# Kernel tuning notes

Measured on AMD Instinct MI355X. Metric: run time of the kernel, lower is better.

## Reference

```python
import jax, jax.numpy as jnp
import numpy as np

EPS = 1e-8  # torch.cosine_similarity default eps


def setup_inputs() -> dict:
    key = jax.random.key(0)
    ks = jax.random.split(key, 6)
    B, U, P, H = 256, 128, 64, 768
    utt_output = jax.random.normal(ks[0], (U, B, H), dtype=jnp.float32)
    pheno_output = jax.random.normal(ks[1], (P, B, H), dtype=jnp.float32)
    # Conv1d(in=U, out=U, kernel=P) weight: [out, in, kernel]
    w_utt = jax.random.normal(ks[2], (U, U, P), dtype=jnp.float32) / np.sqrt(U * P)
    b_utt = jax.random.normal(ks[3], (U,), dtype=jnp.float32) * 0.01
    # Conv1d(in=P, out=P, kernel=U) weight: [out, in, kernel]
    w_pheno = jax.random.normal(ks[4], (P, P, U), dtype=jnp.float32) / np.sqrt(P * U)
    b_pheno = jax.random.normal(ks[5], (P,), dtype=jnp.float32) * 0.01
    return {"utt_output": utt_output, "pheno_output": pheno_output,
            "w_utt": w_utt, "b_utt": b_utt, "w_pheno": w_pheno, "b_pheno": b_pheno}


def reference(utt_output, pheno_output, w_utt, b_utt, w_pheno, b_pheno):
    # [len, B, H] -> [B, len, H]
    u = jnp.swapaxes(utt_output, 0, 1)    # [B, U, H]
    p = jnp.swapaxes(pheno_output, 0, 1)  # [B, P, H]
    # cosine similarity matrix c[b,i,j] = <u_i, p_j> / (max(|u_i|,eps)*max(|p_j|,eps))
    un = u / jnp.maximum(jnp.linalg.norm(u, axis=-1, keepdims=True), EPS)
    pn = p / jnp.maximum(jnp.linalg.norm(p, axis=-1, keepdims=True), EPS)
    c = jnp.einsum('buh,bph->bup', un, pn)  # [B, U, P]
    # Conv1d with kernel covering the full width -> output length 1, i.e. an einsum
    row_logits = jnp.einsum('bup,oup->bo', c, w_utt) + b_utt        # [B, U]
    col_logits = jnp.einsum('bup,opu->bo', c, w_pheno) + b_pheno    # [B, P]
    row_attention = jax.nn.softmax(row_logits, axis=-1)
    col_attention = jax.nn.softmax(col_logits, axis=-1)
    return row_attention, col_attention
```

## Files before the change

### kernel.cpp

```cpp
#include <hip/hip_runtime.h>
#include <stdint.h>

#define Bn 256
#define Un 128
#define Pn 64
#define Hn 768
#define Ototal 192
#define KC 16

#define LDU 40
#define LDB 72

typedef short s4v __attribute__((ext_vector_type(4)));
typedef short s8v __attribute__((ext_vector_type(8)));
typedef float f4v __attribute__((ext_vector_type(4)));

__device__ __forceinline__ short f2bf(float x) {
  union { float f; uint32_t u; } c; c.f = x;
  uint32_t r = (c.u + 0x7fffu + ((c.u >> 16) & 1u)) >> 16;
  return (short)(r & 0xffffu);
}

__global__ void __launch_bounds__(256) convW(const float* __restrict__ w_utt,
                                             const float* __restrict__ w_ph,
                                             ushort* __restrict__ Wbf) {
  __shared__ float tile[64 * 129];
  const int bx = blockIdx.x;
  const int t = threadIdx.x;
  if (bx < 4096) {
    int idx = bx * 256 + t;
    Wbf[idx] = (ushort)f2bf(w_utt[idx]);
    return;
  }
  const int oc = bx - 4096;
  const float* src = w_ph + (size_t)oc * 8192;
#pragma unroll
  for (int itr = 0; itr < 8; ++itr) {
    int idx = itr * 1024 + t * 4;
    int j = idx >> 7, i = idx & 127;
    float4 v = *(const float4*)(src + idx);
    tile[j * 129 + i + 0] = v.x;
    tile[j * 129 + i + 1] = v.y;
    tile[j * 129 + i + 2] = v.z;
    tile[j * 129 + i + 3] = v.w;
  }
  __syncthreads();
  const size_t obase = (size_t)(128 + oc) * 8192;
#pragma unroll
  for (int itr = 0; itr < 8; ++itr) {
    int k = itr * 1024 + t * 4;
    int i = k >> 6, j = k & 63;
    s4v o4 = { f2bf(tile[(j + 0) * 129 + i]),
               f2bf(tile[(j + 1) * 129 + i]),
               f2bf(tile[(j + 2) * 129 + i]),
               f2bf(tile[(j + 3) * 129 + i]) };
    *(s4v*)&Wbf[obase + k] = o4;
  }
}

__global__ void __launch_bounds__(512) phaseA(const float* __restrict__ utt,
                                              const float* __restrict__ ph,
                                              ushort* __restrict__ Cbf) {
  const int bx = blockIdx.x;
  const int b = bx >> 1, half = bx & 1;
  const int t = threadIdx.x;
  const int w = t >> 6, l = t & 63;

  __shared__ short uA[64 * LDU];
  __shared__ short pB[64 * LDU];
  __shared__ float s_inu[64];
  __shared__ float s_inp[64];

  const int r  = t >> 3;
  const int cc = (t & 7) * 4;

  const size_t rstride = (size_t)Bn * Hn;
  const float* ubase = utt + (size_t)b * Hn + (size_t)(half * 64 + r) * rstride + cc;
  const float* pbase = ph  + (size_t)b * Hn + (size_t)r * rstride + cc;

  float4 ru = *(const float4*)ubase;
  float4 rp = *(const float4*)pbase;

  float ssu = 0.f, ssp = 0.f;
  f4v zero4 = {0.f, 0.f, 0.f, 0.f};
  f4v acc0 = zero4, acc1 = zero4;

  const int m  = l & 15;
  const int ko = (l >> 4) * 8;
  const int it = w & 3;
  const int jp = w >> 2;
  const int lw = r * LDU + (t & 7) * 4;

  const short* ab = &uA[(it * 16 + m) * LDU + ko];
  const short* bb = &pB[(jp * 32 + m) * LDU + ko];

  for (int c = 0; c < 24; ++c) {
    __syncthreads();
    float4 a = ru, p0 = rp;
    ssu += a.x*a.x + a.y*a.y + a.z*a.z + a.w*a.w;
    ssp += p0.x*p0.x + p0.y*p0.y + p0.z*p0.z + p0.w*p0.w;
    s4v au = { f2bf(a.x),  f2bf(a.y),  f2bf(a.z),  f2bf(a.w)  };
    s4v pp = { f2bf(p0.x), f2bf(p0.y), f2bf(p0.z), f2bf(p0.w) };
    *(s4v*)&uA[lw] = au;
    *(s4v*)&pB[lw] = pp;
    __syncthreads();
    if (c < 23) {
      ru = *(const float4*)(ubase + (c + 1) * 32);
      rp = *(const float4*)(pbase + (c + 1) * 32);
    }
    s8v af  = *(const s8v*)ab;
    s8v bf0 = *(const s8v*)bb;
    s8v bf1 = *(const s8v*)(bb + 16 * LDU);
    acc0 = __builtin_amdgcn_mfma_f32_16x16x32_bf16(af, bf0, acc0, 0, 0, 0);
    acc1 = __builtin_amdgcn_mfma_f32_16x16x32_bf16(af, bf1, acc1, 0, 0, 0);
  }

  ssu += __shfl_xor(ssu, 4); ssu += __shfl_xor(ssu, 2); ssu += __shfl_xor(ssu, 1);
  ssp += __shfl_xor(ssp, 4); ssp += __shfl_xor(ssp, 2); ssp += __shfl_xor(ssp, 1);
  if ((t & 7) == 0) {
    s_inu[r] = 1.f / fmaxf(sqrtf(ssu), 1e-8f);
    s_inp[r] = 1.f / fmaxf(sqrtf(ssp), 1e-8f);
  }
  __syncthreads();

  const int cl = l & 15;
  const int rq = (l >> 4) * 4;
#pragma unroll
  for (int jt = 0; jt < 2; ++jt) {
    int j = jp * 32 + jt * 16 + cl;
    float sj = s_inp[j];
    f4v a = (jt == 0) ? acc0 : acc1;
#pragma unroll
    for (int rr = 0; rr < 4; ++rr) {
      int il = it * 16 + rq + rr;
      float v = a[rr] * s_inu[il] * sj;
      Cbf[((size_t)b * Un + half * 64 + il) * Pn + j] = (ushort)f2bf(v);
    }
  }
}

__global__ void __launch_bounds__(256) phaseB(const ushort* __restrict__ Cbf,
                                              const ushort* __restrict__ Wbf,
                                              float* __restrict__ partial) {
  const int kc = blockIdx.x;
  const int mt = blockIdx.y;
  const int nt = blockIdx.z;
  const int t = threadIdx.x;
  const int w = t >> 6, l = t & 63;

  __shared__ short Ab[64 * LDB];
  __shared__ short Bb[64 * LDB];

  const int row = t >> 2;
  const int k16 = (t & 3) * 16;

  f4v zero4 = {0.f, 0.f, 0.f, 0.f};
  f4v acc[4] = {zero4, zero4, zero4, zero4};

  const ushort* Ag = Cbf + (size_t)(mt * 64 + row) * 8192 + kc * 512 + k16;
  const ushort* Bg = Wbf + (size_t)(nt * 64 + row) * 8192 + kc * 512 + k16;
  const int m  = l & 15;
  const int ko = (l >> 4) * 8;

  for (int c = 0; c < 8; ++c) {
    s8v av0 = *(const s8v*)(Ag + c * 64);
    s8v av1 = *(const s8v*)(Ag + c * 64 + 8);
    s8v bv0 = *(const s8v*)(Bg + c * 64);
    s8v bv1 = *(const s8v*)(Bg + c * 64 + 8);
    __syncthreads();
    *(s8v*)&Ab[row * LDB + k16]     = av0;
    *(s8v*)&Ab[row * LDB + k16 + 8] = av1;
    *(s8v*)&Bb[row * LDB + k16]     = bv0;
    *(s8v*)&Bb[row * LDB + k16 + 8] = bv1;
    __syncthreads();
#pragma unroll
    for (int ks = 0; ks < 2; ++ks) {
      s8v af = *(const s8v*)&Ab[(16 * w + m) * LDB + ks * 32 + ko];
#pragma unroll
      for (int jt = 0; jt < 4; ++jt) {
        s8v bf = *(const s8v*)&Bb[(16 * jt + m) * LDB + ks * 32 + ko];
        acc[jt] = __builtin_amdgcn_mfma_f32_16x16x32_bf16(af, bf, acc[jt], 0, 0, 0);
      }
    }
  }

  const int rq = (l >> 4) * 4;
#pragma unroll
  for (int jt = 0; jt < 4; ++jt) {
    int og = nt * 64 + 16 * jt + (l & 15);
#pragma unroll
    for (int r = 0; r < 4; ++r) {
      int bg = mt * 64 + 16 * w + rq + r;
      partial[((size_t)kc * Bn + bg) * Ototal + og] = acc[jt][r];
    }
  }
}

__global__ void __launch_bounds__(192) phaseC(const float* __restrict__ partial,
                                              const float* __restrict__ b_utt,
                                              const float* __restrict__ b_ph,
                                              float* __restrict__ out) {
  const int b = blockIdx.x;
  const int t = threadIdx.x;
  const int w = t >> 6, l = t & 63;

  float v = 0.f;
#pragma unroll
  for (int kc = 0; kc < KC; ++kc)
    v += partial[((size_t)kc * Bn + b) * Ototal + t];
  v += (t < Un) ? b_utt[t] : b_ph[t - Un];

  __shared__ float red[3];
  float mx = v;
  for (int o = 32; o >= 1; o >>= 1) mx = fmaxf(mx, __shfl_xor(mx, o));
  if (l == 0) red[w] = mx;
  __syncthreads();
  float gmax = (t < Un) ? fmaxf(red[0], red[1]) : red[2];
  float e = expf(v - gmax);
  float s = e;
  for (int o = 32; o >= 1; o >>= 1) s += __shfl_xor(s, o);
  __syncthreads();
  if (l == 0) red[w] = s;
  __syncthreads();
  float gs = (t < Un) ? (red[0] + red[1]) : red[2];
  float r = e / gs;
  if (t < Un) out[(size_t)b * Un + t] = r;
  else        out[(size_t)Bn * Un + (size_t)b * Pn + (t - Un)] = r;
}

extern "C" void kernel_launch(void* const* d_in, const int* in_sizes, int n_in,
                              void* d_out, int out_size, void* d_ws, size_t ws_size,
                              hipStream_t stream) {
  const float* utt   = (const float*)d_in[0];
  const float* ph    = (const float*)d_in[1];
  const float* w_utt = (const float*)d_in[2];
  const float* b_utt = (const float*)d_in[3];
  const float* w_ph  = (const float*)d_in[4];
  const float* b_ph  = (const float*)d_in[5];

  char* ws = (char*)d_ws;
  ushort* Cbf     = (ushort*)(ws);
  ushort* Wbf     = (ushort*)(ws + 4194304);
  float*  partial = (float*)(ws + 7340032);

  convW <<<dim3(4096 + 64), dim3(256), 0, stream>>>(w_utt, w_ph, Wbf);
  phaseA<<<dim3(2 * Bn), dim3(512), 0, stream>>>(utt, ph, Cbf);
  phaseB<<<dim3(KC, 4, 3), dim3(256), 0, stream>>>(Cbf, Wbf, partial);
  phaseC<<<dim3(Bn), dim3(192), 0, stream>>>(partial, b_utt, b_ph, (float*)d_out);
}
```

Baseline: 211.5 us.

## Load MFMA operands directly from global memory in phaseA, dropping LDS staging

phaseA now has each lane load its MFMA A/B fragments straight from global memory as float4 pairs and convert them to bf16 in registers. This removes the shared-memory tiles and the two barriers per K-chunk. Each wave computes a 16x64 tile with four accumulators, and the norms come from cross-lane shuffles instead of LDS. Block size drops to 256 and the block index mapping changes to b-major. The cost is that the pheno rows are re-read by each of the four waves and by both halves, which raises global/L2 traffic and register pressure.

```diff
diff --git a/kernel.cpp b/kernel.cpp
--- a/kernel.cpp
+++ b/kernel.cpp
@@ -8,7 +8,6 @@
 #define Ototal 192
 #define KC 16
 
-#define LDU 40
 #define LDB 72
 
 typedef short s4v __attribute__((ext_vector_type(4)));
@@ -19,6 +18,17 @@
   union { float f; uint32_t u; } c; c.f = x;
   uint32_t r = (c.u + 0x7fffu + ((c.u >> 16) & 1u)) >> 16;
   return (short)(r & 0xffffu);
+}
+
+__device__ __forceinline__ float dot4(float4 v) {
+  return v.x * v.x + v.y * v.y + v.z * v.z + v.w * v.w;
+}
+
+__device__ __forceinline__ s8v pack8(float4 x, float4 y) {
+  s8v r;
+  r[0] = f2bf(x.x); r[1] = f2bf(x.y); r[2] = f2bf(x.z); r[3] = f2bf(x.w);
+  r[4] = f2bf(y.x); r[5] = f2bf(y.y); r[6] = f2bf(y.z); r[7] = f2bf(y.w);
+  return r;
 }
 
 __global__ void __launch_bounds__(256) convW(const float* __restrict__ w_utt,
@@ -58,84 +68,84 @@
   }
 }
 
-__global__ void __launch_bounds__(512) phaseA(const float* __restrict__ utt,
+__global__ void __launch_bounds__(256) phaseA(const float* __restrict__ utt,
                                               const float* __restrict__ ph,
                                               ushort* __restrict__ Cbf) {
   const int bx = blockIdx.x;
-  const int b = bx >> 1, half = bx & 1;
+  const int b = bx & 255;
+  const int half = bx >> 8;
   const int t = threadIdx.x;
   const int w = t >> 6, l = t & 63;
-
-  __shared__ short uA[64 * LDU];
-  __shared__ short pB[64 * LDU];
-  __shared__ float s_inu[64];
-  __shared__ float s_inp[64];
-
-  const int r  = t >> 3;
-  const int cc = (t & 7) * 4;
-
-  const size_t rstride = (size_t)Bn * Hn;
-  const float* ubase = utt + (size_t)b * Hn + (size_t)(half * 64 + r) * rstride + cc;
-  const float* pbase = ph  + (size_t)b * Hn + (size_t)r * rstride + cc;
-
-  float4 ru = *(const float4*)ubase;
-  float4 rp = *(const float4*)pbase;
-
-  float ssu = 0.f, ssp = 0.f;
-  f4v zero4 = {0.f, 0.f, 0.f, 0.f};
-  f4v acc0 = zero4, acc1 = zero4;
-
   const int m  = l & 15;
   const int ko = (l >> 4) * 8;
-  const int it = w & 3;
-  const int jp = w >> 2;
-  const int lw = r * LDU + (t & 7) * 4;
-
-  const short* ab = &uA[(it * 16 + m) * LDU + ko];
-  const short* bb = &pB[(jp * 32 + m) * LDU + ko];
-
+
+  const size_t RS = (size_t)Bn * Hn;
+
+  const float* ua  = utt + (size_t)(half * 64 + w * 16 + m) * RS
+                         + (size_t)b * Hn + ko;
+  const float* pa0 = ph  + (size_t)m * RS + (size_t)b * Hn + ko;
+  const float* pa1 = pa0 + (size_t)16 * RS;
+  const float* pa2 = pa0 + (size_t)32 * RS;
+  const float* pa3 = pa0 + (size_t)48 * RS;
+
+  f4v zero4 = {0.f, 0.f, 0.f, 0.f};
+  f4v acc0 = zero4, acc1 = zero4, acc2 = zero4, acc3 = zero4;
+  float ssu = 0.f, ssp0 = 0.f, ssp1 = 0.f, ssp2 = 0.f, ssp3 = 0.f;
+
+#pragma unroll 2
   for (int c = 0; c < 24; ++c) {
-    __syncthreads();
-    float4 a = ru, p0 = rp;
-    ssu += a.x*a.x + a.y*a.y + a.z*a.z + a.w*a.w;
-    ssp += p0.x*p0.x + p0.y*p0.y + p0.z*p0.z + p0.w*p0.w;
-    s4v au = { f2bf(a.x),  f2bf(a.y),  f2bf(a.z),  f2bf(a.w)  };
-    s4v pp = { f2bf(p0.x), f2bf(p0.y), f2bf(p0.z), f2bf(p0.w) };
-    *(s4v*)&uA[lw] = au;
-    *(s4v*)&pB[lw] = pp;
-    __syncthreads();
-    if (c < 23) {
-      ru = *(const float4*)(ubase + (c + 1) * 32);
-      rp = *(const float4*)(pbase + (c + 1) * 32);
-    }
-    s8v af  = *(const s8v*)ab;
-    s8v bf0 = *(const s8v*)bb;
-    s8v bf1 = *(const s8v*)(bb + 16 * LDU);
-    acc0 = __builtin_amdgcn_mfma_f32_16x16x32_bf16(af, bf0, acc0, 0, 0, 0);
-    acc1 = __builtin_amdgcn_mfma_f32_16x16x32_bf16(af, bf1, acc1, 0, 0, 0);
-  }
-
-  ssu += __shfl_xor(ssu, 4); ssu += __shfl_xor(ssu, 2); ssu += __shfl_xor(ssu, 1);
-  ssp += __shfl_xor(ssp, 4); ssp += __shfl_xor(ssp, 2); ssp += __shfl_xor(ssp, 1);
-  if ((t & 7) == 0) {
-    s_inu[r] = 1.f / fmaxf(sqrtf(ssu), 1e-8f);
-    s_inp[r] = 1.f / fmaxf(sqrtf(ssp), 1e-8f);
-  }
-  __syncthreads();
-
-  const int cl = l & 15;
+    const int o = c * 32;
+    float4 a0  = *(const float4*)(ua  + o);
+    float4 a1  = *(const float4*)(ua  + o + 4);
+    float4 q00 = *(const float4*)(pa0 + o);
+    float4 q01 = *(const float4*)(pa0 + o + 4);
+    float4 q10 = *(const float4*)(pa1 + o);
+    float4 q11 = *(const float4*)(pa1 + o + 4);
+    float4 q20 = *(const float4*)(pa2 + o);
+    float4 q21 = *(const float4*)(pa2 + o + 4);
+    float4 q30 = *(const float4*)(pa3 + o);
+    float4 q31 = *(const float4*)(pa3 + o + 4);
+
+    ssu  += dot4(a0)  + dot4(a1);
+    ssp0 += dot4(q00) + dot4(q01);
+    ssp1 += dot4(q10) + dot4(q11);
+    ssp2 += dot4(q20) + dot4(q21);
+    ssp3 += dot4(q30) + dot4(q31);
+
+    s8v af = pack8(a0, a1);
+    acc0 = __builtin_amdgcn_mfma_f32_16x16x32_bf16(af, pack8(q00, q01), acc0, 0, 0, 0);
+    acc1 = __builtin_amdgcn_mfma_f32_16x16x32_bf16(af, pack8(q10, q11), acc1, 0, 0, 0);
+    acc2 = __builtin_amdgcn_mfma_f32_16x16x32_bf16(af, pack8(q20, q21), acc2, 0, 0, 0);
+    acc3 = __builtin_amdgcn_mfma_f32_16x16x32_bf16(af, pack8(q30, q31), acc3, 0, 0, 0);
+  }
+
+  ssu  += __shfl_xor(ssu, 16);  ssu  += __shfl_xor(ssu, 32);
+  ssp0 += __shfl_xor(ssp0, 16); ssp0 += __shfl_xor(ssp0, 32);
+  ssp1 += __shfl_xor(ssp1, 16); ssp1 += __shfl_xor(ssp1, 32);
+  ssp2 += __shfl_xor(ssp2, 16); ssp2 += __shfl_xor(ssp2, 32);
+  ssp3 += __shfl_xor(ssp3, 16); ssp3 += __shfl_xor(ssp3, 32);
+
+  const float ip0 = 1.f / fmaxf(sqrtf(ssp0), 1e-8f);
+  const float ip1 = 1.f / fmaxf(sqrtf(ssp1), 1e-8f);
+  const float ip2 = 1.f / fmaxf(sqrtf(ssp2), 1e-8f);
+  const float ip3 = 1.f / fmaxf(sqrtf(ssp3), 1e-8f);
+
   const int rq = (l >> 4) * 4;
-#pragma unroll
-  for (int jt = 0; jt < 2; ++jt) {
-    int j = jp * 32 + jt * 16 + cl;
-    float sj = s_inp[j];
-    f4v a = (jt == 0) ? acc0 : acc1;
-#pragma unroll
-    for (int rr = 0; rr < 4; ++rr) {
-      int il = it * 16 + rq + rr;
-      float v = a[rr] * s_inu[il] * sj;
-      Cbf[((size_t)b * Un + half * 64 + il) * Pn + j] = (ushort)f2bf(v);
-    }
+  float inu[4];
+#pragma unroll
+  for (int r = 0; r < 4; ++r) {
+    float su = __shfl(ssu, rq + r);
+    inu[r] = 1.f / fmaxf(sqrtf(su), 1e-8f);
+  }
+
+  const size_t cbase = ((size_t)b * Un + half * 64 + w * 16) * Pn;
+#pragma unroll
+  for (int r = 0; r < 4; ++r) {
+    int row = rq + r;
+    Cbf[cbase + (size_t)row * Pn +  0 + m] = (ushort)f2bf(acc0[r] * inu[r] * ip0);
+    Cbf[cbase + (size_t)row * Pn + 16 + m] = (ushort)f2bf(acc1[r] * inu[r] * ip1);
+    Cbf[cbase + (size_t)row * Pn + 32 + m] = (ushort)f2bf(acc2[r] * inu[r] * ip2);
+    Cbf[cbase + (size_t)row * Pn + 48 + m] = (ushort)f2bf(acc3[r] * inu[r] * ip3);
   }
 }
 
@@ -244,7 +254,7 @@
   float*  partial = (float*)(ws + 7340032);
 
   convW <<<dim3(4096 + 64), dim3(256), 0, stream>>>(w_utt, w_ph, Wbf);
-  phaseA<<<dim3(2 * Bn), dim3(512), 0, stream>>>(utt, ph, Cbf);
+  phaseA<<<dim3(2 * Bn), dim3(256), 0, stream>>>(utt, ph, Cbf);
   phaseB<<<dim3(KC, 4, 3), dim3(256), 0, stream>>>(Cbf, Wbf, partial);
   phaseC<<<dim3(Bn), dim3(192), 0, stream>>>(partial, b_utt, b_ph, (float*)d_out);
 }
```

Result: slower. 237.3 us (+12.2%).

## Fuse weight conversion into phaseA kernel and double-buffer LDS tiles

Applied to the files above, without the earlier changes.

Merges the bf16 weight conversion kernel into the cosine-similarity kernel as extra blocks of one launch, removing a kernel launch and letting weight conversion overlap with the similarity computation. The similarity loop now double-buffers its LDS tiles, so the next chunk is converted and stored while MFMAs run on the current one, which halves the barriers per iteration. The cost is a larger fixed shared allocation (the transpose tile) for every block, which may lower occupancy of the phaseA blocks.

```diff
diff --git a/kernel.cpp b/kernel.cpp
--- a/kernel.cpp
+++ b/kernel.cpp
@@ -21,55 +21,62 @@
   return (short)(r & 0xffffu);
 }
 
-__global__ void __launch_bounds__(256) convW(const float* __restrict__ w_utt,
-                                             const float* __restrict__ w_ph,
-                                             ushort* __restrict__ Wbf) {
-  __shared__ float tile[64 * 129];
+__device__ __forceinline__ float dot4(float4 v) {
+  return v.x * v.x + v.y * v.y + v.z * v.z + v.w * v.w;
+}
+
+__global__ void __launch_bounds__(512) phaseAW(const float* __restrict__ utt,
+                                               const float* __restrict__ ph,
+                                               ushort* __restrict__ Cbf,
+                                               const float* __restrict__ w_utt,
+                                               const float* __restrict__ w_ph,
+                                               ushort* __restrict__ Wbf) {
+  __shared__ __align__(16) float smemf[64 * 129];
+  char* smem = (char*)smemf;
   const int bx = blockIdx.x;
   const int t = threadIdx.x;
-  if (bx < 4096) {
-    int idx = bx * 256 + t;
-    Wbf[idx] = (ushort)f2bf(w_utt[idx]);
+
+  if (bx >= 512) {
+    if (bx < 2560) {
+      int idx = (bx - 512) * 512 + t;
+      Wbf[idx] = (ushort)f2bf(w_utt[idx]);
+      return;
+    }
+    float* tile = smemf;
+    const int oc = bx - 2560;
+    const float* src = w_ph + (size_t)oc * 8192;
+#pragma unroll
+    for (int itr = 0; itr < 4; ++itr) {
+      int idx = itr * 2048 + t * 4;
+      int j = idx >> 7, i = idx & 127;
+      float4 v = *(const float4*)(src + idx);
+      tile[j * 129 + i + 0] = v.x;
+      tile[j * 129 + i + 1] = v.y;
+      tile[j * 129 + i + 2] = v.z;
+      tile[j * 129 + i + 3] = v.w;
+    }
+    __syncthreads();
+    const size_t obase = (size_t)(128 + oc) * 8192;
+#pragma unroll
+    for (int itr = 0; itr < 4; ++itr) {
+      int k = itr * 2048 + t * 4;
+      int i = k >> 6, j = k & 63;
+      s4v o4 = { f2bf(tile[(j + 0) * 129 + i]),
+                 f2bf(tile[(j + 1) * 129 + i]),
+                 f2bf(tile[(j + 2) * 129 + i]),
+                 f2bf(tile[(j + 3) * 129 + i]) };
+      *(s4v*)&Wbf[obase + k] = o4;
+    }
     return;
   }
-  const int oc = bx - 4096;
-  const float* src = w_ph + (size_t)oc * 8192;
-#pragma unroll
-  for (int itr = 0; itr < 8; ++itr) {
-    int idx = itr * 1024 + t * 4;
-    int j = idx >> 7, i = idx & 127;
-    float4 v = *(const float4*)(src + idx);
-    tile[j * 129 + i + 0] = v.x;
-    tile[j * 129 + i + 1] = v.y;
-    tile[j * 129 + i + 2] = v.z;
-    tile[j * 129 + i + 3] = v.w;
-  }
-  __syncthreads();
-  const size_t obase = (size_t)(128 + oc) * 8192;
-#pragma unroll
-  for (int itr = 0; itr < 8; ++itr) {
-    int k = itr * 1024 + t * 4;
-    int i = k >> 6, j = k & 63;
-    s4v o4 = { f2bf(tile[(j + 0) * 129 + i]),
-               f2bf(tile[(j + 1) * 129 + i]),
-               f2bf(tile[(j + 2) * 129 + i]),
-               f2bf(tile[(j + 3) * 129 + i]) };
-    *(s4v*)&Wbf[obase + k] = o4;
-  }
-}
-
-__global__ void __launch_bounds__(512) phaseA(const float* __restrict__ utt,
-                                              const float* __restrict__ ph,
-                                              ushort* __restrict__ Cbf) {
-  const int bx = blockIdx.x;
+
+  short (*uA)[64 * LDU] = (short (*)[64 * LDU])(smem);
+  short (*pB)[64 * LDU] = (short (*)[64 * LDU])(smem + 10240);
+  float* s_inu = (float*)(smem + 20480);
+  float* s_inp = (float*)(smem + 20736);
+
   const int b = bx >> 1, half = bx & 1;
-  const int t = threadIdx.x;
   const int w = t >> 6, l = t & 63;
-
-  __shared__ short uA[64 * LDU];
-  __shared__ short pB[64 * LDU];
-  __shared__ float s_inu[64];
-  __shared__ float s_inp[64];
 
   const int r  = t >> 3;
   const int cc = (t & 7) * 4;
@@ -77,42 +84,51 @@
   const size_t rstride = (size_t)Bn * Hn;
   const float* ubase = utt + (size_t)b * Hn + (size_t)(half * 64 + r) * rstride + cc;
   const float* pbase = ph  + (size_t)b * Hn + (size_t)r * rstride + cc;
-
-  float4 ru = *(const float4*)ubase;
-  float4 rp = *(const float4*)pbase;
-
-  float ssu = 0.f, ssp = 0.f;
-  f4v zero4 = {0.f, 0.f, 0.f, 0.f};
-  f4v acc0 = zero4, acc1 = zero4;
 
   const int m  = l & 15;
   const int ko = (l >> 4) * 8;
   const int it = w & 3;
   const int jp = w >> 2;
   const int lw = r * LDU + (t & 7) * 4;
-
-  const short* ab = &uA[(it * 16 + m) * LDU + ko];
-  const short* bb = &pB[(jp * 32 + m) * LDU + ko];
-
-  for (int c = 0; c < 24; ++c) {
-    __syncthreads();
-    float4 a = ru, p0 = rp;
-    ssu += a.x*a.x + a.y*a.y + a.z*a.z + a.w*a.w;
-    ssp += p0.x*p0.x + p0.y*p0.y + p0.z*p0.z + p0.w*p0.w;
+  const int fo = (it * 16 + m) * LDU + ko;
+  const int go = (jp * 32 + m) * LDU + ko;
+
+  f4v zero4 = {0.f, 0.f, 0.f, 0.f};
+  f4v acc0 = zero4, acc1 = zero4;
+  float ssu = 0.f, ssp = 0.f;
+
+  {
+    float4 a  = *(const float4*)ubase;
+    float4 p0 = *(const float4*)pbase;
+    ssu += dot4(a); ssp += dot4(p0);
     s4v au = { f2bf(a.x),  f2bf(a.y),  f2bf(a.z),  f2bf(a.w)  };
     s4v pp = { f2bf(p0.x), f2bf(p0.y), f2bf(p0.z), f2bf(p0.w) };
-    *(s4v*)&uA[lw] = au;
-    *(s4v*)&pB[lw] = pp;
-    __syncthreads();
+    *(s4v*)&uA[0][lw] = au;
+    *(s4v*)&pB[0][lw] = pp;
+  }
+  __syncthreads();
+
+#pragma unroll 2
+  for (int c = 0; c < 24; ++c) {
+    const int cur = c & 1;
+    float4 nu, np;
     if (c < 23) {
-      ru = *(const float4*)(ubase + (c + 1) * 32);
-      rp = *(const float4*)(pbase + (c + 1) * 32);
-    }
-    s8v af  = *(const s8v*)ab;
-    s8v bf0 = *(const s8v*)bb;
-    s8v bf1 = *(const s8v*)(bb + 16 * LDU);
+      nu = *(const float4*)(ubase + (c + 1) * 32);
+      np = *(const float4*)(pbase + (c + 1) * 32);
+    }
+    s8v af  = *(const s8v*)&uA[cur][fo];
+    s8v bf0 = *(const s8v*)&pB[cur][go];
+    s8v bf1 = *(const s8v*)&pB[cur][go + 16 * LDU];
     acc0 = __builtin_amdgcn_mfma_f32_16x16x32_bf16(af, bf0, acc0, 0, 0, 0);
     acc1 = __builtin_amdgcn_mfma_f32_16x16x32_bf16(af, bf1, acc1, 0, 0, 0);
+    if (c < 23) {
+      ssu += dot4(nu); ssp += dot4(np);
+      s4v au = { f2bf(nu.x), f2bf(nu.y), f2bf(nu.z), f2bf(nu.w) };
+      s4v pp = { f2bf(np.x), f2bf(np.y), f2bf(np.z), f2bf(np.w) };
+      *(s4v*)&uA[cur ^ 1][lw] = au;
+      *(s4v*)&pB[cur ^ 1][lw] = pp;
+    }
+    __syncthreads();
   }
 
   ssu += __shfl_xor(ssu, 4); ssu += __shfl_xor(ssu, 2); ssu += __shfl_xor(ssu, 1);
@@ -243,8 +259,7 @@
   ushort* Wbf     = (ushort*)(ws + 4194304);
   float*  partial = (float*)(ws + 7340032);
 
-  convW <<<dim3(4096 + 64), dim3(256), 0, stream>>>(w_utt, w_ph, Wbf);
-  phaseA<<<dim3(2 * Bn), dim3(512), 0, stream>>>(utt, ph, Cbf);
-  phaseB<<<dim3(KC, 4, 3), dim3(256), 0, stream>>>(Cbf, Wbf, partial);
-  phaseC<<<dim3(Bn), dim3(192), 0, stream>>>(partial, b_utt, b_ph, (float*)d_out);
-}
+  phaseAW<<<dim3(2624), dim3(512), 0, stream>>>(utt, ph, Cbf, w_utt, w_ph, Wbf);
+  phaseB <<<dim3(KC, 4, 3), dim3(256), 0, stream>>>(Cbf, Wbf, partial);
+  phaseC <<<dim3(Bn), dim3(192), 0, stream>>>(partial, b_utt, b_ph, (float*)d_out);
+}
```

New measurement: 208.0 us. About the same (-1.6%).

## Fuse four kernels into one persistent kernel with global atomic barriers

Applied to the files above, without the earlier changes.

Merges the weight conversion, cosine-similarity GEMM, logits GEMM and softmax kernels into a single 512-block kernel. The phases are separated by software grid barriers built on atomic counters, which are zeroed by a memset before launch. This removes three kernel launch gaps and the tail idle time between dependent stages. The phaseB GEMM now stages its A and B tiles with all 512 threads splitting the loads. In exchange it depends on all 512 blocks being co-resident (deadlock otherwise), adds barrier spin cost, and falls back to using the output buffer as the counter when the workspace is too small.

```diff
diff --git a/kernel.cpp b/kernel.cpp
--- a/kernel.cpp
+++ b/kernel.cpp
@@ -7,6 +7,7 @@
 #define Hn 768
 #define Ototal 192
 #define KC 16
+#define NBLK 512
 
 #define LDU 40
 #define LDB 72
@@ -21,211 +22,227 @@
   return (short)(r & 0xffffu);
 }
 
-__global__ void __launch_bounds__(256) convW(const float* __restrict__ w_utt,
-                                             const float* __restrict__ w_ph,
-                                             ushort* __restrict__ Wbf) {
-  __shared__ float tile[64 * 129];
+__device__ __forceinline__ float dot4(float4 v) {
+  return v.x * v.x + v.y * v.y + v.z * v.z + v.w * v.w;
+}
+
+__device__ __forceinline__ void gbar(unsigned* c, int t) {
+  __threadfence();
+  __syncthreads();
+  if (t == 0) {
+    __hip_atomic_fetch_add(c, 1u, __ATOMIC_ACQ_REL, __HIP_MEMORY_SCOPE_AGENT);
+    while (__hip_atomic_load(c, __ATOMIC_ACQUIRE, __HIP_MEMORY_SCOPE_AGENT)
+           < (unsigned)NBLK)
+      __builtin_amdgcn_s_sleep(8);
+  }
+  __syncthreads();
+  __threadfence();
+}
+
+__global__ void __launch_bounds__(512, 4) mega(
+    const float* __restrict__ utt, const float* __restrict__ ph,
+    const float* __restrict__ w_utt, const float* __restrict__ w_ph,
+    const float* __restrict__ b_utt, const float* __restrict__ b_ph,
+    ushort* __restrict__ Cbf, ushort* __restrict__ Wbf,
+    float* __restrict__ partial, float* __restrict__ out,
+    unsigned* __restrict__ ctr) {
+  __shared__ __align__(16) char smem[33536];
   const int bx = blockIdx.x;
   const int t = threadIdx.x;
-  if (bx < 4096) {
-    int idx = bx * 256 + t;
-    Wbf[idx] = (ushort)f2bf(w_utt[idx]);
-    return;
-  }
-  const int oc = bx - 4096;
-  const float* src = w_ph + (size_t)oc * 8192;
-#pragma unroll
-  for (int itr = 0; itr < 8; ++itr) {
-    int idx = itr * 1024 + t * 4;
-    int j = idx >> 7, i = idx & 127;
-    float4 v = *(const float4*)(src + idx);
-    tile[j * 129 + i + 0] = v.x;
-    tile[j * 129 + i + 1] = v.y;
-    tile[j * 129 + i + 2] = v.z;
-    tile[j * 129 + i + 3] = v.w;
-  }
-  __syncthreads();
-  const size_t obase = (size_t)(128 + oc) * 8192;
-#pragma unroll
-  for (int itr = 0; itr < 8; ++itr) {
-    int k = itr * 1024 + t * 4;
-    int i = k >> 6, j = k & 63;
-    s4v o4 = { f2bf(tile[(j + 0) * 129 + i]),
-               f2bf(tile[(j + 1) * 129 + i]),
-               f2bf(tile[(j + 2) * 129 + i]),
-               f2bf(tile[(j + 3) * 129 + i]) };
-    *(s4v*)&Wbf[obase + k] = o4;
-  }
-}
-
-__global__ void __launch_bounds__(512) phaseA(const float* __restrict__ utt,
-                                              const float* __restrict__ ph,
-                                              ushort* __restrict__ Cbf) {
-  const int bx = blockIdx.x;
-  const int b = bx >> 1, half = bx & 1;
-  const int t = threadIdx.x;
   const int w = t >> 6, l = t & 63;
-
-  __shared__ short uA[64 * LDU];
-  __shared__ short pB[64 * LDU];
-  __shared__ float s_inu[64];
-  __shared__ float s_inp[64];
-
-  const int r  = t >> 3;
-  const int cc = (t & 7) * 4;
-
-  const size_t rstride = (size_t)Bn * Hn;
-  const float* ubase = utt + (size_t)b * Hn + (size_t)(half * 64 + r) * rstride + cc;
-  const float* pbase = ph  + (size_t)b * Hn + (size_t)r * rstride + cc;
-
-  float4 ru = *(const float4*)ubase;
-  float4 rp = *(const float4*)pbase;
-
-  float ssu = 0.f, ssp = 0.f;
-  f4v zero4 = {0.f, 0.f, 0.f, 0.f};
-  f4v acc0 = zero4, acc1 = zero4;
-
-  const int m  = l & 15;
-  const int ko = (l >> 4) * 8;
-  const int it = w & 3;
-  const int jp = w >> 2;
-  const int lw = r * LDU + (t & 7) * 4;
-
-  const short* ab = &uA[(it * 16 + m) * LDU + ko];
-  const short* bb = &pB[(jp * 32 + m) * LDU + ko];
-
-  for (int c = 0; c < 24; ++c) {
-    __syncthreads();
-    float4 a = ru, p0 = rp;
-    ssu += a.x*a.x + a.y*a.y + a.z*a.z + a.w*a.w;
-    ssp += p0.x*p0.x + p0.y*p0.y + p0.z*p0.z + p0.w*p0.w;
-    s4v au = { f2bf(a.x),  f2bf(a.y),  f2bf(a.z),  f2bf(a.w)  };
-    s4v pp = { f2bf(p0.x), f2bf(p0.y), f2bf(p0.z), f2bf(p0.w) };
-    *(s4v*)&uA[lw] = au;
-    *(s4v*)&pB[lw] = pp;
-    __syncthreads();
-    if (c < 23) {
-      ru = *(const float4*)(ubase + (c + 1) * 32);
-      rp = *(const float4*)(pbase + (c + 1) * 32);
-    }
-    s8v af  = *(const s8v*)ab;
-    s8v bf0 = *(const s8v*)bb;
-    s8v bf1 = *(const s8v*)(bb + 16 * LDU);
-    acc0 = __builtin_amdgcn_mfma_f32_16x16x32_bf16(af, bf0, acc0, 0, 0, 0);
-    acc1 = __builtin_amdgcn_mfma_f32_16x16x32_bf16(af, bf1, acc1, 0, 0, 0);
-  }
-
-  ssu += __shfl_xor(ssu, 4); ssu += __shfl_xor(ssu, 2); ssu += __shfl_xor(ssu, 1);
-  ssp += __shfl_xor(ssp, 4); ssp += __shfl_xor(ssp, 2); ssp += __shfl_xor(ssp, 1);
-  if ((t & 7) == 0) {
-    s_inu[r] = 1.f / fmaxf(sqrtf(ssu), 1e-8f);
-    s_inp[r] = 1.f / fmaxf(sqrtf(ssp), 1e-8f);
-  }
-  __syncthreads();
-
-  const int cl = l & 15;
-  const int rq = (l >> 4) * 4;
-#pragma unroll
-  for (int jt = 0; jt < 2; ++jt) {
-    int j = jp * 32 + jt * 16 + cl;
-    float sj = s_inp[j];
-    f4v a = (jt == 0) ? acc0 : acc1;
-#pragma unroll
-    for (int rr = 0; rr < 4; ++rr) {
-      int il = it * 16 + rq + rr;
-      float v = a[rr] * s_inu[il] * sj;
-      Cbf[((size_t)b * Un + half * 64 + il) * Pn + j] = (ushort)f2bf(v);
-    }
-  }
-}
-
-__global__ void __launch_bounds__(256) phaseB(const ushort* __restrict__ Cbf,
-                                              const ushort* __restrict__ Wbf,
-                                              float* __restrict__ partial) {
-  const int kc = blockIdx.x;
-  const int mt = blockIdx.y;
-  const int nt = blockIdx.z;
-  const int t = threadIdx.x;
-  const int w = t >> 6, l = t & 63;
-
-  __shared__ short Ab[64 * LDB];
-  __shared__ short Bb[64 * LDB];
-
-  const int row = t >> 2;
-  const int k16 = (t & 3) * 16;
-
-  f4v zero4 = {0.f, 0.f, 0.f, 0.f};
-  f4v acc[4] = {zero4, zero4, zero4, zero4};
-
-  const ushort* Ag = Cbf + (size_t)(mt * 64 + row) * 8192 + kc * 512 + k16;
-  const ushort* Bg = Wbf + (size_t)(nt * 64 + row) * 8192 + kc * 512 + k16;
-  const int m  = l & 15;
-  const int ko = (l >> 4) * 8;
-
-  for (int c = 0; c < 8; ++c) {
-    s8v av0 = *(const s8v*)(Ag + c * 64);
-    s8v av1 = *(const s8v*)(Ag + c * 64 + 8);
-    s8v bv0 = *(const s8v*)(Bg + c * 64);
-    s8v bv1 = *(const s8v*)(Bg + c * 64 + 8);
-    __syncthreads();
-    *(s8v*)&Ab[row * LDB + k16]     = av0;
-    *(s8v*)&Ab[row * LDB + k16 + 8] = av1;
-    *(s8v*)&Bb[row * LDB + k16]     = bv0;
-    *(s8v*)&Bb[row * LDB + k16 + 8] = bv1;
-    __syncthreads();
-#pragma unroll
-    for (int ks = 0; ks < 2; ++ks) {
-      s8v af = *(const s8v*)&Ab[(16 * w + m) * LDB + ks * 32 + ko];
-#pragma unroll
-      for (int jt = 0; jt < 4; ++jt) {
-        s8v bf = *(const s8v*)&Bb[(16 * jt + m) * LDB + ks * 32 + ko];
-        acc[jt] = __builtin_amdgcn_mfma_f32_16x16x32_bf16(af, bf, acc[jt], 0, 0, 0);
-      }
-    }
-  }
-
-  const int rq = (l >> 4) * 4;
-#pragma unroll
-  for (int jt = 0; jt < 4; ++jt) {
-    int og = nt * 64 + 16 * jt + (l & 15);
-#pragma unroll
-    for (int r = 0; r < 4; ++r) {
-      int bg = mt * 64 + 16 * w + rq + r;
-      partial[((size_t)kc * Bn + bg) * Ototal + og] = acc[jt][r];
-    }
-  }
-}
-
-__global__ void __launch_bounds__(192) phaseC(const float* __restrict__ partial,
-                                              const float* __restrict__ b_utt,
-                                              const float* __restrict__ b_ph,
-                                              float* __restrict__ out) {
-  const int b = blockIdx.x;
-  const int t = threadIdx.x;
-  const int w = t >> 6, l = t & 63;
-
-  float v = 0.f;
-#pragma unroll
-  for (int kc = 0; kc < KC; ++kc)
-    v += partial[((size_t)kc * Bn + b) * Ototal + t];
-  v += (t < Un) ? b_utt[t] : b_ph[t - Un];
-
-  __shared__ float red[3];
-  float mx = v;
-  for (int o = 32; o >= 1; o >>= 1) mx = fmaxf(mx, __shfl_xor(mx, o));
-  if (l == 0) red[w] = mx;
-  __syncthreads();
-  float gmax = (t < Un) ? fmaxf(red[0], red[1]) : red[2];
-  float e = expf(v - gmax);
-  float s = e;
-  for (int o = 32; o >= 1; o >>= 1) s += __shfl_xor(s, o);
-  __syncthreads();
-  if (l == 0) red[w] = s;
-  __syncthreads();
-  float gs = (t < Un) ? (red[0] + red[1]) : red[2];
-  float r = e / gs;
-  if (t < Un) out[(size_t)b * Un + t] = r;
-  else        out[(size_t)Bn * Un + (size_t)b * Pn + (t - Un)] = r;
+  const f4v zero4 = {0.f, 0.f, 0.f, 0.f};
+
+  {
+    int base = bx * 2048 + t * 4;
+    float4 v = *(const float4*)(w_utt + base);
+    s4v o = { f2bf(v.x), f2bf(v.y), f2bf(v.z), f2bf(v.w) };
+    *(s4v*)&Wbf[base] = o;
+  }
+  if (bx < 64) {
+    float* tile = (float*)smem;
+    const float* src = w_ph + (size_t)bx * 8192;
+#pragma unroll
+    for (int itr = 0; itr < 4; ++itr) {
+      int idx = itr * 2048 + t * 4;
+      int j = idx >> 7, i = idx & 127;
+      float4 v = *(const float4*)(src + idx);
+      tile[j * 129 + i + 0] = v.x;
+      tile[j * 129 + i + 1] = v.y;
+      tile[j * 129 + i + 2] = v.z;
+      tile[j * 129 + i + 3] = v.w;
+    }
+    __syncthreads();
+    const size_t obase = (size_t)(128 + bx) * 8192;
+#pragma unroll
+    for (int itr = 0; itr < 4; ++itr) {
+      int k = itr * 2048 + t * 4;
+      int i = k >> 6, j = k & 63;
+      s4v o4 = { f2bf(tile[(j + 0) * 129 + i]),
+                 f2bf(tile[(j + 1) * 129 + i]),
+                 f2bf(tile[(j + 2) * 129 + i]),
+                 f2bf(tile[(j + 3) * 129 + i]) };
+      *(s4v*)&Wbf[obase + k] = o4;
+    }
+    __syncthreads();
+  }
+
+  {
+    short* uA = (short*)smem;
+    short* pB = (short*)(smem + 5120);
+    float* s_inu = (float*)(smem + 10240);
+    float* s_inp = (float*)(smem + 10496);
+
+    const int b = bx >> 1, half = bx & 1;
+    const int r  = t >> 3;
+    const int cc = (t & 7) * 4;
+
+    const size_t rstride = (size_t)Bn * Hn;
+    const float* ubase = utt + (size_t)b * Hn + (size_t)(half * 64 + r) * rstride + cc;
+    const float* pbase = ph  + (size_t)b * Hn + (size_t)r * rstride + cc;
+
+    float4 ru = *(const float4*)ubase;
+    float4 rp = *(const float4*)pbase;
+
+    float ssu = 0.f, ssp = 0.f;
+    f4v acc0 = zero4, acc1 = zero4;
+
+    const int m  = l & 15;
+    const int ko = (l >> 4) * 8;
+    const int it = w & 3;
+    const int jp = w >> 2;
+    const int lw = r * LDU + cc;
+    const short* ab = &uA[(it * 16 + m) * LDU + ko];
+    const short* bb = &pB[(jp * 32 + m) * LDU + ko];
+
+    for (int c = 0; c < 24; ++c) {
+      __syncthreads();
+      float4 a = ru, p0 = rp;
+      ssu += dot4(a);
+      ssp += dot4(p0);
+      s4v au = { f2bf(a.x),  f2bf(a.y),  f2bf(a.z),  f2bf(a.w)  };
+      s4v pp = { f2bf(p0.x), f2bf(p0.y), f2bf(p0.z), f2bf(p0.w) };
+      *(s4v*)&uA[lw] = au;
+      *(s4v*)&pB[lw] = pp;
+      __syncthreads();
+      if (c < 23) {
+        ru = *(const float4*)(ubase + (c + 1) * 32);
+        rp = *(const float4*)(pbase + (c + 1) * 32);
+      }
+      s8v af  = *(const s8v*)ab;
+      s8v bf0 = *(const s8v*)bb;
+      s8v bf1 = *(const s8v*)(bb + 16 * LDU);
+      acc0 = __builtin_amdgcn_mfma_f32_16x16x32_bf16(af, bf0, acc0, 0, 0, 0);
+      acc1 = __builtin_amdgcn_mfma_f32_16x16x32_bf16(af, bf1, acc1, 0, 0, 0);
+    }
+
+    ssu += __shfl_xor(ssu, 4); ssu += __shfl_xor(ssu, 2); ssu += __shfl_xor(ssu, 1);
+    ssp += __shfl_xor(ssp, 4); ssp += __shfl_xor(ssp, 2); ssp += __shfl_xor(ssp, 1);
+    if ((t & 7) == 0) {
+      s_inu[r] = 1.f / fmaxf(sqrtf(ssu), 1e-8f);
+      s_inp[r] = 1.f / fmaxf(sqrtf(ssp), 1e-8f);
+    }
+    __syncthreads();
+
+    const int cl = l & 15;
+    const int rq = (l >> 4) * 4;
+#pragma unroll
+    for (int jt = 0; jt < 2; ++jt) {
+      int j = jp * 32 + jt * 16 + cl;
+      float sj = s_inp[j];
+      f4v a = (jt == 0) ? acc0 : acc1;
+#pragma unroll
+      for (int rr = 0; rr < 4; ++rr) {
+        int il = it * 16 + rq + rr;
+        float v = a[rr] * s_inu[il] * sj;
+        Cbf[((size_t)b * Un + half * 64 + il) * Pn + j] = (ushort)f2bf(v);
+      }
+    }
+  }
+
+  gbar(ctr + 0, t);
+
+  if (bx < KC * 12) {
+    const int kc = bx & 15, mt = (bx >> 4) & 3, nt = bx >> 6;
+    short* Ab = (short*)smem;
+    short* Bb = (short*)(smem + 9216);
+
+    const int sB  = t >> 8;
+    const int tb  = t & 255;
+    const int row = tb >> 2;
+    const int k16 = (tb & 3) * 16;
+    const ushort* G = (sB ? Wbf + (size_t)(nt * 64 + row) * 8192
+                          : Cbf + (size_t)(mt * 64 + row) * 8192) + kc * 512 + k16;
+    short* S = (sB ? Bb : Ab) + row * LDB + k16;
+
+    const int m  = l & 15;
+    const int ko = (l >> 4) * 8;
+    const int mtile = w & 3;
+    const int jh    = w >> 2;
+    f4v acc[2] = {zero4, zero4};
+
+    for (int c = 0; c < 8; ++c) {
+      s8v v0 = *(const s8v*)(G + c * 64);
+      s8v v1 = *(const s8v*)(G + c * 64 + 8);
+      __syncthreads();
+      *(s8v*)S = v0;
+      *(s8v*)(S + 8) = v1;
+      __syncthreads();
+#pragma unroll
+      for (int ks = 0; ks < 2; ++ks) {
+        s8v af = *(const s8v*)&Ab[(16 * mtile + m) * LDB + ks * 32 + ko];
+#pragma unroll
+        for (int jt = 0; jt < 2; ++jt) {
+          s8v bf = *(const s8v*)&Bb[(jh * 32 + jt * 16 + m) * LDB + ks * 32 + ko];
+          acc[jt] = __builtin_amdgcn_mfma_f32_16x16x32_bf16(af, bf, acc[jt], 0, 0, 0);
+        }
+      }
+    }
+
+    const int rq = (l >> 4) * 4;
+#pragma unroll
+    for (int jt = 0; jt < 2; ++jt) {
+      int og = nt * 64 + jh * 32 + jt * 16 + (l & 15);
+#pragma unroll
+      for (int rr = 0; rr < 4; ++rr) {
+        int bg = mt * 64 + mtile * 16 + rq + rr;
+        partial[((size_t)kc * Bn + bg) * Ototal + og] = acc[jt][rr];
+      }
+    }
+  }
+
+  gbar(ctr + 1, t);
+
+  if (bx < Bn) {
+    float* red = (float*)smem;
+    const bool act = t < Ototal;
+    float v = 0.f, e = 0.f;
+    if (act) {
+#pragma unroll
+      for (int kc = 0; kc < KC; ++kc)
+        v += partial[((size_t)kc * Bn + bx) * Ototal + t];
+      v += (t < Un) ? b_utt[t] : b_ph[t - Un];
+    }
+    float mx = v;
+    for (int o = 32; o >= 1; o >>= 1) mx = fmaxf(mx, __shfl_xor(mx, o));
+    if (act && l == 0) red[w] = mx;
+    __syncthreads();
+    float gmax = 0.f;
+    if (act) {
+      gmax = (t < Un) ? fmaxf(red[0], red[1]) : red[2];
+      e = expf(v - gmax);
+    }
+    float s = act ? e : 0.f;
+    for (int o = 32; o >= 1; o >>= 1) s += __shfl_xor(s, o);
+    __syncthreads();
+    if (act && l == 0) red[w] = s;
+    __syncthreads();
+    if (act) {
+      float gs = (t < Un) ? (red[0] + red[1]) : red[2];
+      float r = e / gs;
+      if (t < Un) out[(size_t)bx * Un + t] = r;
+      else        out[(size_t)Bn * Un + (size_t)bx * Pn + (t - Un)] = r;
+    }
+  }
 }
 
 extern "C" void kernel_launch(void* const* d_in, const int* in_sizes, int n_in,
@@ -243,8 +260,12 @@
   ushort* Wbf     = (ushort*)(ws + 4194304);
   float*  partial = (float*)(ws + 7340032);
 
-  convW <<<dim3(4096 + 64), dim3(256), 0, stream>>>(w_utt, w_ph, Wbf);
-  phaseA<<<dim3(2 * Bn), dim3(512), 0, stream>>>(utt, ph, Cbf);
-  phaseB<<<dim3(KC, 4, 3), dim3(256), 0, stream>>>(Cbf, Wbf, partial);
-  phaseC<<<dim3(Bn), dim3(192), 0, stream>>>(partial, b_utt, b_ph, (float*)d_out);
-}
+  unsigned* ctr = (ws_size >= 10485760 + 16)
+                      ? (unsigned*)(ws + 10485760)
+                      : (unsigned*)d_out;
+  hipMemsetAsync(ctr, 0, 2 * sizeof(unsigned), stream);
+
+  mega<<<dim3(NBLK), dim3(512), 0, stream>>>(utt, ph, w_utt, w_ph, b_utt, b_ph,
+                                             Cbf, Wbf, partial, (float*)d_out,
+                                             ctr);
+}
```

Result: slower. 605.8 us (+186.4%).
